# Optimization experiments

Hardware: AMD Instinct MI355X
Metric: run time of the kernel (lower is better)

The kernel has to match this reference:

```python
import jax, jax.numpy as jnp
import numpy as np

INPUT, HIDDEN, CLASSES = 4096, 4096, 1000


def setup_inputs() -> dict:
    key = jax.random.key(0)
    kx, kw1, kb1, kw2, kb2 = jax.random.split(key, 5)
    return {
        "x": jax.random.normal(kx, (8192, INPUT), dtype=jnp.float32),
        "fc1_weight": jax.random.normal(kw1, (HIDDEN, INPUT), dtype=jnp.float32),
        "fc1_bias": jax.random.normal(kb1, (HIDDEN,), dtype=jnp.float32),
        "fc2_weight": jax.random.normal(kw2, (CLASSES, HIDDEN), dtype=jnp.float32),
        "fc2_bias": jax.random.normal(kb2, (CLASSES,), dtype=jnp.float32),
    }


def reference(x, fc1_weight, fc1_bias, fc2_weight, fc2_bias):
    # x: [B, INPUT] (module flattens; already flat here)
    hidden = jnp.einsum("bi,hi->bh", x, fc1_weight) + fc1_bias  # [B, H]
    activated = jax.nn.relu(hidden)
    logits = jnp.einsum("bh,ch->bc", activated, fc2_weight) + fc2_bias  # [B, C]
    return jax.nn.softmax(logits, axis=-1)
```

## Files before the change

kernel.cpp:

```cpp
#include <hip/hip_runtime.h>
#include <hip/hip_fp16.h>
#include <stdint.h>

typedef __attribute__((ext_vector_type(8))) _Float16 f16x8;
typedef __attribute__((ext_vector_type(4))) _Float16 f16x4;
typedef __attribute__((ext_vector_type(4))) float f32x4;

__device__ __forceinline__ void split4(const f32x4 v, f16x4 &h, f16x4 &l) {
    #pragma unroll
    for (int i = 0; i < 4; ++i) {
        float a = v[i];
        _Float16 hh = (_Float16)a;
        h[i] = hh;
        l[i] = (_Float16)(a - (float)hh);
    }
}

__global__ __launch_bounds__(256)
void split_rows(const float* __restrict__ src, _Float16* __restrict__ h,
                _Float16* __restrict__ l, int srcRows, long long total4)
{
    const long long stride = (long long)gridDim.x * blockDim.x;
    for (long long i = (long long)blockIdx.x * blockDim.x + threadIdx.x; i < total4; i += stride) {
        const long long e = i << 2;
        const int row = (int)(e >> 12);
        f16x4 hv = {}, lv = {};
        if (row < srcRows) {
            f32x4 v = *(const f32x4*)(src + e);
            split4(v, hv, lv);
        }
        *(f16x4*)(h + e) = hv;
        *(f16x4*)(l + e) = lv;
    }
}


#define BARRIER() __builtin_amdgcn_s_barrier()
#define LGKM0() do { asm volatile("s_waitcnt lgkmcnt(0)" ::: "memory"); __builtin_amdgcn_sched_barrier(0); } while (0)
#define VMC0()  do { asm volatile("s_waitcnt vmcnt(0)"  ::: "memory"); __builtin_amdgcn_sched_barrier(0); } while (0)

__device__ __forceinline__ void gload16(const _Float16* g, _Float16* l) {
    __builtin_amdgcn_global_load_lds(
        (const __attribute__((address_space(1))) void*)g,
        (__attribute__((address_space(3))) void*)l, 16, 0, 0);
}

template<int MI, bool SPLITOUT>
__global__ __launch_bounds__(512, 2)
void gemm3_phase(const _Float16* __restrict__ Agh, const _Float16* __restrict__ Agl,
                 const _Float16* __restrict__ Bgh, const _Float16* __restrict__ Bgl,
                 const float* __restrict__ bias,
                 _Float16* __restrict__ Oh, _Float16* __restrict__ Ol,
                 float* __restrict__ Of, int ldo, int Nstore,
                 int K, int nBM)
{
    extern __shared__ _Float16 lds[];
    constexpr int WROWS = MI * 16;
    constexpr int BM    = MI * 32;
    constexpr int CHA   = MI * 2;
    constexpr int PW    = (2*CHA + 32) / 8;
    constexpr int ALO   = CHA * 512;
    constexpr int BHO   = 2 * CHA * 512;
    constexpr int BUFS  = 2*CHA*512 + 16384;
    constexpr int S1 = (PW == 8) ? 3 : 2;
    constexpr int S2 = (PW == 8) ? 6 : 4;

    const int tid  = threadIdx.x;
    const int lane = tid & 63;
    const int wave = tid >> 6;
    const int wm = wave >> 2;
    const int wn = wave & 3;
    const int fr = lane & 15;
    const int fg = lane >> 4;

    const int nwg  = gridDim.x;
    const int cpx  = nwg >> 3;
    const int orig = blockIdx.x;
    const int swzb = (orig & 7) * cpx + (orig >> 3);
    const int bm = swzb % nBM;
    const int bn = swzb / nBM;
    const int m0 = bm * BM;
    const int n0 = bn * 256;

    const _Float16* gptr[8];
    int loff[8];
    #pragma unroll
    for (int i = 0; i < PW; ++i) {
        const int ch = wave * PW + i;
        int p, q;
        if      (ch < CHA)        { p = 0; q = ch; }
        else if (ch < 2*CHA)      { p = 1; q = ch - CHA; }
        else if (ch < 2*CHA + 16) { p = 2; q = ch - 2*CHA; }
        else                      { p = 3; q = ch - 2*CHA - 16; }
        const int row = q*16 + (lane >> 2);
        const int gc  = (lane & 3) ^ ((row >> 1) & 3);
        const _Float16* plane = (p == 0) ? Agh : (p == 1) ? Agl : (p == 2) ? Bgh : Bgl;
        const size_t grow = (size_t)((p < 2) ? m0 : n0) + row;
        gptr[i] = plane + grow * (size_t)K + gc * 8;
        loff[i] = ((p < 2) ? p * ALO : BHO + (p - 2) * 8192) + q * 512;
    }

    const int swz8 = (fg ^ ((fr >> 1) & 3)) * 8;
    int aoff[MI], boff[4];
    #pragma unroll
    for (int mi = 0; mi < MI; ++mi) aoff[mi] = (wm*WROWS + mi*16 + fr)*32 + swz8;
    #pragma unroll
    for (int ni = 0; ni < 4; ++ni)  boff[ni] = BHO + (wn*64 + ni*16 + fr)*32 + swz8;

    f32x4 acc[MI][4] = {};

    #pragma unroll
    for (int i = 0; i < PW; ++i) { gload16(gptr[i], &lds[loff[i]]); gptr[i] += 32; }
    VMC0(); BARRIER();

    const int NT = K >> 5;
    int bb = 0;
    for (int t = 0; t < NT; ++t) {
        const int  nb = BUFS - bb;
        const bool st = (t < NT - 1);
        f16x8 ah[MI], al[MI], bhf, blf;

#define PHASE(NI, SBEG, SEND, LAST) do {                                              \
        bhf = *(const f16x8*)&lds[bb + boff[NI]];                                     \
        blf = *(const f16x8*)&lds[bb + 8192 + boff[NI]];                              \
        if (st) {                                                                     \
            _Pragma("unroll")                                                         \
            for (int i = (SBEG); i < (SEND); ++i) {                                   \
                gload16(gptr[i], &lds[nb + loff[i]]); gptr[i] += 32;                  \
            }                                                                         \
        }                                                                             \
        BARRIER(); LGKM0();                                                           \
        __builtin_amdgcn_s_setprio(1);                                                \
        _Pragma("unroll")                                                             \
        for (int mi = 0; mi < MI; ++mi) {                                             \
            acc[mi][NI] = __builtin_amdgcn_mfma_f32_16x16x32_f16(ah[mi], bhf, acc[mi][NI], 0, 0, 0); \
            acc[mi][NI] = __builtin_amdgcn_mfma_f32_16x16x32_f16(ah[mi], blf, acc[mi][NI], 0, 0, 0); \
            acc[mi][NI] = __builtin_amdgcn_mfma_f32_16x16x32_f16(al[mi], bhf, acc[mi][NI], 0, 0, 0); \
        }                                                                             \
        __builtin_amdgcn_s_setprio(0);                                                \
        if (LAST) VMC0();                                                             \
        BARRIER();                                                                    \
    } while (0)

        #pragma unroll
        for (int mi = 0; mi < MI; ++mi) {
            ah[mi] = *(const f16x8*)&lds[bb + aoff[mi]];
            al[mi] = *(const f16x8*)&lds[bb + ALO + aoff[mi]];
        }
        PHASE(0, 0, S1, false);
        PHASE(1, S1, S2, false);
        PHASE(2, S2, PW, false);
        PHASE(3, 0, 0, true);
#undef PHASE
        bb = nb;
    }

    #pragma unroll
    for (int ni = 0; ni < 4; ++ni) {
        const int n = n0 + wn*64 + ni*16 + fr;
        if (!SPLITOUT && n >= Nstore) continue;
        const float bv = bias[n];
        #pragma unroll
        for (int mi = 0; mi < MI; ++mi) {
            #pragma unroll
            for (int j = 0; j < 4; ++j) {
                const int m = m0 + wm*WROWS + mi*16 + fg*4 + j;
                float v = acc[mi][ni][j] + bv;
                if (SPLITOUT) {
                    v = fmaxf(v, 0.f);
                    const _Float16 hh = (_Float16)v;
                    Oh[(size_t)m * ldo + n] = hh;
                    Ol[(size_t)m * ldo + n] = (_Float16)(v - (float)hh);
                } else {
                    Of[(size_t)m * ldo + n] = v;
                }
            }
        }
    }
}

#define TILE_M 128
#define TILE_N 128
#define TILE_K 32
#define LDSK   40

template<bool RELU, bool NGUARD>
__global__ __launch_bounds__(256, 2)
void gemm_split3(const float* __restrict__ A, const float* __restrict__ B,
                 const float* __restrict__ bias, float* __restrict__ C,
                 int K, int ldc, int Nreal)
{
    __shared__ _Float16 Ah[TILE_M][LDSK];
    __shared__ _Float16 Al[TILE_M][LDSK];
    __shared__ _Float16 Bh[TILE_N][LDSK];
    __shared__ _Float16 Bl[TILE_N][LDSK];

    const int tid  = threadIdx.x;
    const int lane = tid & 63;
    const int wave = tid >> 6;
    const int wr   = wave >> 1;
    const int wc   = wave & 1;
    const int m0   = blockIdx.x * TILE_M;
    const int n0   = blockIdx.y * TILE_N;
    const int srow = tid >> 3;
    const int scol = (tid & 7) << 2;
    const int fr = lane & 15;
    const int fg = lane >> 4;

    f32x4 acc[4][4] = {};

    for (int kt = 0; kt < K; kt += TILE_K) {
        __syncthreads();
        #pragma unroll
        for (int p = 0; p < 4; ++p) {
            const int row = srow + p * 32;
            f32x4 v = *(const f32x4*)(A + (size_t)(m0 + row) * K + kt + scol);
            f16x4 hv, lv;
            split4(v, hv, lv);
            *(f16x4*)&Ah[row][scol] = hv;
            *(f16x4*)&Al[row][scol] = lv;
        }
        #pragma unroll
        for (int p = 0; p < 4; ++p) {
            const int row = srow + p * 32;
            f32x4 v = {0.f, 0.f, 0.f, 0.f};
            if (!NGUARD || (n0 + row) < Nreal)
                v = *(const f32x4*)(B + (size_t)(n0 + row) * K + kt + scol);
            f16x4 hv, lv;
            split4(v, hv, lv);
            *(f16x4*)&Bh[row][scol] = hv;
            *(f16x4*)&Bl[row][scol] = lv;
        }
        __syncthreads();

        f16x8 ah[4], al[4];
        #pragma unroll
        for (int mi = 0; mi < 4; ++mi) {
            const int r = wr * 64 + mi * 16 + fr;
            ah[mi] = *(const f16x8*)&Ah[r][fg * 8];
            al[mi] = *(const f16x8*)&Al[r][fg * 8];
        }
        #pragma unroll
        for (int ni = 0; ni < 4; ++ni) {
            const int r = wc * 64 + ni * 16 + fr;
            const f16x8 bh = *(const f16x8*)&Bh[r][fg * 8];
            const f16x8 bl = *(const f16x8*)&Bl[r][fg * 8];
            #pragma unroll
            for (int mi = 0; mi < 4; ++mi) {
                acc[mi][ni] = __builtin_amdgcn_mfma_f32_16x16x32_f16(ah[mi], bh, acc[mi][ni], 0, 0, 0);
                acc[mi][ni] = __builtin_amdgcn_mfma_f32_16x16x32_f16(ah[mi], bl, acc[mi][ni], 0, 0, 0);
                acc[mi][ni] = __builtin_amdgcn_mfma_f32_16x16x32_f16(al[mi], bh, acc[mi][ni], 0, 0, 0);
            }
        }
    }

    #pragma unroll
    for (int ni = 0; ni < 4; ++ni) {
        const int n = n0 + wc * 64 + ni * 16 + fr;
        if (NGUARD && n >= Nreal) continue;
        const float bv = bias[n];
        #pragma unroll
        for (int mi = 0; mi < 4; ++mi) {
            #pragma unroll
            for (int j = 0; j < 4; ++j) {
                const int m = m0 + wr * 64 + mi * 16 + fg * 4 + j;
                float val = acc[mi][ni][j] + bv;
                if (RELU) val = fmaxf(val, 0.f);
                C[(size_t)m * ldc + n] = val;
            }
        }
    }
}

__global__ __launch_bounds__(256)
void softmax_rows(float* __restrict__ out, int rows, int cols)
{
    const int lane = threadIdx.x & 63;
    const int row  = blockIdx.x * 4 + (threadIdx.x >> 6);
    if (row >= rows) return;
    float* p = out + (size_t)row * cols;

    float v[16];
    float mx = -3.4e38f;
    #pragma unroll
    for (int j = 0; j < 16; ++j) {
        const int c = lane + j * 64;
        v[j] = (c < cols) ? p[c] : -3.4e38f;
        mx = fmaxf(mx, v[j]);
    }
    #pragma unroll
    for (int off = 32; off > 0; off >>= 1)
        mx = fmaxf(mx, __shfl_xor(mx, off));

    float s = 0.f;
    #pragma unroll
    for (int j = 0; j < 16; ++j) {
        const int c = lane + j * 64;
        const float e = (c < cols) ? __expf(v[j] - mx) : 0.f;
        v[j] = e;
        s += e;
    }
    #pragma unroll
    for (int off = 32; off > 0; off >>= 1)
        s += __shfl_xor(s, off);

    const float inv = 1.f / s;
    #pragma unroll
    for (int j = 0; j < 16; ++j) {
        const int c = lane + j * 64;
        if (c < cols) p[c] = v[j] * inv;
    }
}

extern "C" void kernel_launch(void* const* d_in, const int* in_sizes, int n_in,
                              void* d_out, int out_size, void* d_ws, size_t ws_size,
                              hipStream_t stream)
{
    const float* x  = (const float*)d_in[0];
    const float* w1 = (const float*)d_in[1];
    const float* b1 = (const float*)d_in[2];
    const float* w2 = (const float*)d_in[3];
    const float* b2 = (const float*)d_in[4];
    float* out = (float*)d_out;

    const size_t SZ_X  = (size_t)8192 * 4096 * 2;
    const size_t SZ_W1 = (size_t)4096 * 4096 * 2;
    const size_t SZ_W2 = (size_t)1024 * 4096 * 2;

    size_t off = 0;
    auto take = [&](size_t b) { size_t o = off; off += (b + 255) & ~(size_t)255; return o; };
    const size_t o_xh  = take(SZ_X),  o_xl  = take(SZ_X);
    const size_t o_w1h = take(SZ_W1), o_w1l = take(SZ_W1);
    const size_t o_w2h = take(SZ_W2), o_w2l = take(SZ_W2);
    const size_t o_ah  = take(SZ_X),  o_al  = take(SZ_X);
    const size_t need = off;

    bool attr_ok =
        (hipFuncSetAttribute((const void*)gemm3_phase<8, true>,
                             hipFuncAttributeMaxDynamicSharedMemorySize, 131072) == hipSuccess) &&
        (hipFuncSetAttribute((const void*)gemm3_phase<4, false>,
                             hipFuncAttributeMaxDynamicSharedMemorySize, 131072) == hipSuccess);

    const dim3 blk256(256, 1, 1), blk512(512, 1, 1);

    if (attr_ok && ws_size >= need) {
        char* w = (char*)d_ws;
        _Float16 *xh  = (_Float16*)(w + o_xh),  *xl  = (_Float16*)(w + o_xl);
        _Float16 *w1h = (_Float16*)(w + o_w1h), *w1l = (_Float16*)(w + o_w1l);
        _Float16 *w2h = (_Float16*)(w + o_w2h), *w2l = (_Float16*)(w + o_w2l);
        _Float16 *ath = (_Float16*)(w + o_ah),  *atl = (_Float16*)(w + o_al);

        hipLaunchKernelGGL(split_rows, dim3(2048), blk256, 0, stream, x,  xh,  xl,  8192, (long long)8192 * 1024);
        hipLaunchKernelGGL(split_rows, dim3(2048), blk256, 0, stream, w1, w1h, w1l, 4096, (long long)4096 * 1024);
        hipLaunchKernelGGL(split_rows, dim3(1024), blk256, 0, stream, w2, w2h, w2l, 1000, (long long)1024 * 1024);

        hipLaunchKernelGGL((gemm3_phase<8, true>), dim3(512), blk512, 131072, stream,
                           xh, xl, w1h, w1l, b1, ath, atl, (float*)nullptr, 4096, 4096, 4096, 32);
        hipLaunchKernelGGL((gemm3_phase<4, false>), dim3(256), blk512, 98304, stream,
                           ath, atl, w2h, w2l, b2, (_Float16*)nullptr, (_Float16*)nullptr,
                           out, 1000, 1000, 4096, 64);
        hipLaunchKernelGGL(softmax_rows, dim3(2048), blk256, 0, stream, out, 8192, 1000);
    } else {
        float* act = (float*)d_ws;
        hipLaunchKernelGGL((gemm_split3<true, false>), dim3(64, 32), blk256, 0, stream,
                           x, w1, b1, act, 4096, 4096, 4096);
        hipLaunchKernelGGL((gemm_split3<false, true>), dim3(64, 8), blk256, 0, stream,
                           act, w2, b2, out, 4096, 1000, 1000);
        hipLaunchKernelGGL(softmax_rows, dim3(2048), blk256, 0, stream, out, 8192, 1000);
    }
}
```

Before: 1.036 ms.

## Use fine-grained vmcnt waits so B chunks stream in per MFMA phase

Reassigns the global-to-LDS load chunks so each wave loads its A chunks first and then one B sub-tile per N-phase. The full vmcnt(0) drain at the end of each K-step is replaced by partial vmcnt waits, so each phase waits only for the chunk it consumes next and later chunks keep arriving during MFMA work. The final K-step is peeled into its own block that issues no loads and drains the counter step by step. Correctness now depends on load issue order matching the vmcnt thresholds, and on each wave's barrier-protected wait covering the B chunks that the other waves read.

```diff
diff --git a/kernel.cpp b/kernel.cpp
--- a/kernel.cpp
+++ b/kernel.cpp
@@ -37,7 +37,11 @@
 
 #define BARRIER() __builtin_amdgcn_s_barrier()
 #define LGKM0() do { asm volatile("s_waitcnt lgkmcnt(0)" ::: "memory"); __builtin_amdgcn_sched_barrier(0); } while (0)
-#define VMC0()  do { asm volatile("s_waitcnt vmcnt(0)"  ::: "memory"); __builtin_amdgcn_sched_barrier(0); } while (0)
+
+template<int N> __device__ __forceinline__ void VMCNT() {
+    asm volatile("s_waitcnt vmcnt(%0)" :: "n"(N) : "memory");
+    __builtin_amdgcn_sched_barrier(0);
+}
 
 __device__ __forceinline__ void gload16(const _Float16* g, _Float16* l) {
     __builtin_amdgcn_global_load_lds(
@@ -59,11 +63,10 @@
     constexpr int BM    = MI * 32;
     constexpr int CHA   = MI * 2;
     constexpr int PW    = (2*CHA + 32) / 8;
+    constexpr int NA    = PW - 4;
     constexpr int ALO   = CHA * 512;
     constexpr int BHO   = 2 * CHA * 512;
     constexpr int BUFS  = 2*CHA*512 + 16384;
-    constexpr int S1 = (PW == 8) ? 3 : 2;
-    constexpr int S2 = (PW == 8) ? 6 : 4;
 
     const int tid  = threadIdx.x;
     const int lane = tid & 63;
@@ -86,12 +89,15 @@
     int loff[8];
     #pragma unroll
     for (int i = 0; i < PW; ++i) {
-        const int ch = wave * PW + i;
         int p, q;
-        if      (ch < CHA)        { p = 0; q = ch; }
-        else if (ch < 2*CHA)      { p = 1; q = ch - CHA; }
-        else if (ch < 2*CHA + 16) { p = 2; q = ch - 2*CHA; }
-        else                      { p = 3; q = ch - 2*CHA - 16; }
+        if (i < NA) {
+            const int j = wave * NA + i;
+            p = j / CHA; q = j % CHA;
+        } else {
+            const int ni = i - NA;
+            q = ni + (wave & 3) * 4;
+            p = 2 + (wave >> 2);
+        }
         const int row = q*16 + (lane >> 2);
         const int gc  = (lane & 3) ^ ((row >> 1) & 3);
         const _Float16* plane = (p == 0) ? Agh : (p == 1) ? Agl : (p == 2) ? Bgh : Bgl;
@@ -111,23 +117,17 @@
 
     #pragma unroll
     for (int i = 0; i < PW; ++i) { gload16(gptr[i], &lds[loff[i]]); gptr[i] += 32; }
-    VMC0(); BARRIER();
+    VMCNT<3>(); BARRIER();
 
     const int NT = K >> 5;
     int bb = 0;
-    for (int t = 0; t < NT; ++t) {
-        const int  nb = BUFS - bb;
-        const bool st = (t < NT - 1);
-        f16x8 ah[MI], al[MI], bhf, blf;
-
-#define PHASE(NI, SBEG, SEND, LAST) do {                                              \
+
+#define PH(NI, IB, IE, WAIT) do {                                                     \
         bhf = *(const f16x8*)&lds[bb + boff[NI]];                                     \
         blf = *(const f16x8*)&lds[bb + 8192 + boff[NI]];                              \
-        if (st) {                                                                     \
-            _Pragma("unroll")                                                         \
-            for (int i = (SBEG); i < (SEND); ++i) {                                   \
-                gload16(gptr[i], &lds[nb + loff[i]]); gptr[i] += 32;                  \
-            }                                                                         \
+        _Pragma("unroll")                                                             \
+        for (int i = (IB); i < (IE); ++i) {                                           \
+            gload16(gptr[i], &lds[nb + loff[i]]); gptr[i] += 32;                      \
         }                                                                             \
         BARRIER(); LGKM0();                                                           \
         __builtin_amdgcn_s_setprio(1);                                                \
@@ -138,22 +138,39 @@
             acc[mi][NI] = __builtin_amdgcn_mfma_f32_16x16x32_f16(al[mi], bhf, acc[mi][NI], 0, 0, 0); \
         }                                                                             \
         __builtin_amdgcn_s_setprio(0);                                                \
-        if (LAST) VMC0();                                                             \
+        WAIT;                                                                         \
         BARRIER();                                                                    \
     } while (0)
 
+    for (int t = 0; t < NT - 1; ++t) {
+        const int nb = BUFS - bb;
+        f16x8 ah[MI], al[MI], bhf, blf;
         #pragma unroll
         for (int mi = 0; mi < MI; ++mi) {
             ah[mi] = *(const f16x8*)&lds[bb + aoff[mi]];
             al[mi] = *(const f16x8*)&lds[bb + ALO + aoff[mi]];
         }
-        PHASE(0, 0, S1, false);
-        PHASE(1, S1, S2, false);
-        PHASE(2, S2, PW, false);
-        PHASE(3, 0, 0, true);
-#undef PHASE
+        PH(0, 0,    NA,   VMCNT<PW-2>());
+        PH(1, NA,   NA+2, VMCNT<PW-1>());
+        PH(2, NA+2, PW,   VMCNT<PW>());
+        PH(3, 0,    0,    VMCNT<3>());
         bb = nb;
     }
+    {
+        const int nb = BUFS - bb;
+        f16x8 ah[MI], al[MI], bhf, blf;
+        #pragma unroll
+        for (int mi = 0; mi < MI; ++mi) {
+            ah[mi] = *(const f16x8*)&lds[bb + aoff[mi]];
+            al[mi] = *(const f16x8*)&lds[bb + ALO + aoff[mi]];
+        }
+        PH(0, 0, 0, VMCNT<2>());
+        PH(1, 0, 0, VMCNT<1>());
+        PH(2, 0, 0, VMCNT<0>());
+        PH(3, 0, 0, );
+        (void)nb;
+    }
+#undef PH
 
     #pragma unroll
     for (int ni = 0; ni < 4; ++ni) {
```

Measured after the change: 1.013 ms. 2.2% less time.
